# Optimization experiments

Measured on AMD Instinct MI355X. Metric: run time of the kernel, lower is better.

## Reference

```python
import jax, jax.numpy as jnp
import numpy as np
import math

E = 64          # embed_size
S = 64          # max_seq_len (mask hard-codes seq==64)
H = 8           # num_heads
DH = E // H     # 8
DFF = 4 * E     # 256
V = 32000       # vocab_size
B = 64          # batch


def _pos_encoding():
    position = np.arange(0, S, dtype=np.float32)[:, None]
    div_term = np.exp(np.arange(0, E, 2, dtype=np.float32) * -(math.log(10000.0) / E))
    pe = np.zeros((S, E), dtype=np.float32)
    pe[:, 0::2] = np.sin(position * div_term)
    pe[:, 1::2] = np.cos(position * div_term)
    return jnp.asarray(pe)


def layernorm(x, g, b, eps=1e-5):
    mu = jnp.mean(x, -1, keepdims=True)
    var = jnp.mean((x - mu) ** 2, -1, keepdims=True)
    return (x - mu) * jax.lax.rsqrt(var + eps) * g + b


def round4(x):
    return jnp.round(x * 1e4) / 1e4


def setup_inputs() -> dict:
    key = jax.random.key(0)
    ks = jax.random.split(key, 16)
    n = lambda k, sh, s=0.05: jax.random.normal(k, sh, dtype=jnp.float32) * s
    return {
        "x": jax.random.randint(ks[0], (B, S), 0, V),
        "emb": n(ks[1], (V, E), 1.0),
        "pe": _pos_encoding(),
        # per-head q/k/v weights concatenated: [E, H*DH] == [E, E], no bias
        "wq": n(ks[2], (E, E)), "wk": n(ks[3], (E, E)), "wv": n(ks[4], (E, E)),
        "g_h": jnp.ones((E,)), "b_h": jnp.zeros((E,)),           # MHA internal LayerNorm
        "wo": n(ks[5], (E, E)), "bo": jnp.zeros((E,)),           # MHA output linear
        "g1": jnp.ones((E,)), "bt1": jnp.zeros((E,)),            # norm1
        "w1": n(ks[6], (E, DFF)), "b1f": jnp.zeros((DFF,)),      # ffn fc1
        "w2": n(ks[7], (DFF, E)), "b2f": jnp.zeros((E,)),        # ffn fc2
        "g2": jnp.ones((E,)), "bt2": jnp.zeros((E,)),            # norm2
        "gf": jnp.ones((E,)), "bf": jnp.zeros((E,)),             # final norm
        "wout": n(ks[8], (E, V)), "bout": jnp.zeros((V,)),       # final linear
    }


def reference(x, emb, pe, wq, wk, wv, g_h, b_h, wo, bo, g1, bt1,
              w1, b1f, w2, b2f, g2, bt2, gf, bf, wout, bout):
    # embedding + positional encoding (dropout = identity in eval)
    h = emb[x] + pe[:S]                              # [B,S,E]

    # --- multi-head attention (per-head linears fused as one GEMM each) ---
    q = (h @ wq).reshape(B, S, H, DH)
    k = (h @ wk).reshape(B, S, H, DH)
    v = (h @ wv).reshape(B, S, H, DH)
    scores = jnp.einsum('bshd,bthd->bhst', q, k) / math.sqrt(DH)
    causal = jnp.tril(jnp.ones((S, S), dtype=bool))
    scores = jnp.where(causal, scores, -jnp.inf)
    attn = jax.nn.softmax(scores, axis=-1)
    ho = round4(jnp.einsum('bhst,bthd->bshd', attn, v))  # per-head round(decimals=4)
    concat = ho.reshape(B, S, E)
    attn_out = jnp.round(layernorm(concat, g_h, b_h) @ wo + bo)  # round to integers

    # --- transformer block residual/norm/ffn ---
    h = layernorm(h + attn_out, g1, bt1)
    ffn = jax.nn.relu(h @ w1 + b1f) @ w2 + b2f
    h = round4(layernorm(h + ffn, g2, bt2))

    # --- final norm, vocab projection, softmax, round ---
    logits = layernorm(h, gf, bf) @ wout + bout       # [B,S,V]
    probs = jax.nn.softmax(logits, axis=-1)
    return jnp.round(probs)
```

## Files before the change

kernel.cpp:

```cpp
#include <hip/hip_runtime.h>
#include <hip/hip_bf16.h>
#include <math.h>

#define EMB 64
#define SEQ 64
#define NH 8
#define DFF 256
#define VOC 32000
#define BATCH 64

using bf16_t = __hip_bfloat16;
typedef __bf16 bf16x8 __attribute__((ext_vector_type(8)));
typedef float f32x4 __attribute__((ext_vector_type(4)));

#define WOUTT_OFF 0
#define HBF_OFF   4194304
#define GSUM_OFF  (4194304 + 524288)
#define GMAX_OFF  (GSUM_OFF + 16384)
#define H_OFF     (GMAX_OFF + 32768)
#define Q_OFF     (H_OFF + 1048576)
#define K_OFF     (Q_OFF + 1048576)
#define V_OFF     (K_OFF + 1048576)
#define HO_OFF    (V_OFF + 1048576)

__device__ inline unsigned long long packmax(float f, int i) {
  unsigned u = __float_as_uint(f);
  u = (u & 0x80000000u) ? ~u : (u | 0x80000000u);
  return ((unsigned long long)u << 32) | (unsigned)i;
}

__device__ inline float rsum16(float s) {
  s += __shfl_xor(s, 1, 16);
  s += __shfl_xor(s, 2, 16);
  s += __shfl_xor(s, 4, 16);
  s += __shfl_xor(s, 8, 16);
  return s;
}

__device__ inline void gemm64g(const float* __restrict__ in, const float* __restrict__ W,
                               float* __restrict__ out, int t) {
  int i = t >> 2, j0 = (t & 3) * 16;
  float acc[16];
#pragma unroll
  for (int j = 0; j < 16; ++j) acc[j] = 0.f;
#pragma unroll 2
  for (int k = 0; k < 64; ++k) {
    float a = in[i * 65 + k];
    const float4* wr = (const float4*)(W + k * 64 + j0);
    float4 w0 = wr[0], w1v = wr[1], w2v = wr[2], w3v = wr[3];
    acc[0] += a * w0.x;   acc[1] += a * w0.y;   acc[2] += a * w0.z;   acc[3] += a * w0.w;
    acc[4] += a * w1v.x;  acc[5] += a * w1v.y;  acc[6] += a * w1v.z;  acc[7] += a * w1v.w;
    acc[8] += a * w2v.x;  acc[9] += a * w2v.y;  acc[10] += a * w2v.z; acc[11] += a * w2v.w;
    acc[12] += a * w3v.x; acc[13] += a * w3v.y; acc[14] += a * w3v.z; acc[15] += a * w3v.w;
  }
#pragma unroll
  for (int j = 0; j < 16; ++j) out[(size_t)i * 64 + j0 + j] = acc[j];
}

__global__ __launch_bounds__(256) void k_qkv(
    const int* __restrict__ x, const float* __restrict__ emb, const float* __restrict__ pe,
    const float* __restrict__ wq, const float* __restrict__ wk, const float* __restrict__ wv,
    const float* __restrict__ wout, bf16_t* __restrict__ woutT,
    float* __restrict__ H, float* __restrict__ Q, float* __restrict__ K,
    float* __restrict__ V, float* __restrict__ gsums,
    unsigned long long* __restrict__ gmax, float* __restrict__ outp) {
  const int t = threadIdx.x;
  __shared__ float sm[64 * 65];

  if (blockIdx.x >= 564) {
    const int bid = blockIdx.x - 564;
    f32x4 z = {0.f, 0.f, 0.f, 0.f};
    f32x4* o4 = (f32x4*)outp + (size_t)bid * 32000;
    for (int i = t; i < 32000; i += 256) o4[i] = z;
    return;
  }

  if (blockIdx.x >= 64) {
    int v0 = (blockIdx.x - 64) * 64;
    for (int idx = t; idx < 4096; idx += 256) {
      int e = idx >> 6, c = idx & 63;
      sm[e * 65 + c] = wout[(size_t)e * VOC + v0 + c];
    }
    __syncthreads();
    for (int idx = t; idx < 4096; idx += 256) {
      int c = idx >> 6, e = idx & 63;
      woutT[(size_t)(v0 + c) * 64 + e] = __float2bfloat16(sm[e * 65 + c]);
    }
    return;
  }

  const int b = blockIdx.x;
  if (t < 64) {
    gsums[b * 64 + t] = 0.f;
    gmax[b * 64 + t] = 0ULL;
  }
  for (int idx = t; idx < 4096; idx += 256) {
    int i = idx >> 6, e = idx & 63;
    int tok = x[b * 64 + i];
    float v = emb[(size_t)tok * 64 + e] + pe[i * 64 + e];
    sm[i * 65 + e] = v;
    H[((size_t)b * 64 + i) * 64 + e] = v;
  }
  __syncthreads();
  gemm64g(sm, wq, Q + (size_t)b * 4096, t);
  gemm64g(sm, wk, K + (size_t)b * 4096, t);
  gemm64g(sm, wv, V + (size_t)b * 4096, t);
}

__global__ __launch_bounds__(256) void k_attn(const float* __restrict__ Q,
                                              const float* __restrict__ K,
                                              const float* __restrict__ V,
                                              float* __restrict__ HO) {
  const int b = blockIdx.x, h = blockIdx.y;
  const int t = threadIdx.x;
  __shared__ float Qh[64 * 8], Kh[64 * 8], Vh[64 * 8];
  __shared__ float SC[64 * 65];
  const size_t base = (size_t)b * 4096 + h * 8;

  for (int idx = t; idx < 512; idx += 256) {
    int i = idx >> 3, d = idx & 7;
    Qh[i * 8 + d] = Q[base + (size_t)i * 64 + d];
    Kh[i * 8 + d] = K[base + (size_t)i * 64 + d];
    Vh[i * 8 + d] = V[base + (size_t)i * 64 + d];
  }
  __syncthreads();

  const float scale = 0.35355339059327373f;
  const int i = t >> 2, jb = t & 3;
  float qv[8];
#pragma unroll
  for (int d = 0; d < 8; ++d) qv[d] = Qh[i * 8 + d];

  float sv[16];
  float m = -INFINITY;
#pragma unroll
  for (int jj = 0; jj < 16; ++jj) {
    int j = jb * 16 + jj;
    float s;
    if (j <= i) {
      s = 0.f;
#pragma unroll
      for (int d = 0; d < 8; ++d) s += qv[d] * Kh[j * 8 + d];
      s *= scale;
    } else {
      s = -INFINITY;
    }
    sv[jj] = s;
    m = fmaxf(m, s);
  }
  m = fmaxf(m, __shfl_xor(m, 1, 4));
  m = fmaxf(m, __shfl_xor(m, 2, 4));
  float sum = 0.f;
#pragma unroll
  for (int jj = 0; jj < 16; ++jj) {
    float e2 = __expf(sv[jj] - m);
    sv[jj] = e2;
    sum += e2;
  }
  sum += __shfl_xor(sum, 1, 4);
  sum += __shfl_xor(sum, 2, 4);
  float inv = 1.f / sum;
#pragma unroll
  for (int jj = 0; jj < 16; ++jj) SC[i * 65 + jb * 16 + jj] = sv[jj] * inv;
  __syncthreads();

  for (int idx = t; idx < 512; idx += 256) {
    int ii = idx >> 3, d = idx & 7;
    float o = 0.f;
    for (int j = 0; j < 64; ++j) o += SC[ii * 65 + j] * Vh[j * 8 + d];
    HO[base + (size_t)ii * 64 + d] = rintf(o * 1e4f) / 1e4f;
  }
}

__global__ __launch_bounds__(256) void k_ffn(
    const float* __restrict__ H, const float* __restrict__ HO,
    const float* __restrict__ g_h, const float* __restrict__ b_h,
    const float* __restrict__ wo, const float* __restrict__ bo,
    const float* __restrict__ g1, const float* __restrict__ bt1,
    const float* __restrict__ w1, const float* __restrict__ b1f,
    const float* __restrict__ w2, const float* __restrict__ b2f,
    const float* __restrict__ g2, const float* __restrict__ bt2,
    const float* __restrict__ gf, const float* __restrict__ bf_,
    bf16_t* __restrict__ hbf) {
  const int t = threadIdx.x;
  const int r0 = blockIdx.x * 16;
  const int i = t >> 4, l = t & 15;
  const int e0 = l * 4;
  const size_t row = (size_t)(r0 + i) * 64;
  __shared__ float T1[16 * 65];
  __shared__ float T2[16 * 65];
  __shared__ float H1[16 * 65];
  __shared__ float M[16 * 260];

  {
    float4 hv = *(const float4*)(HO + row + e0);
    float mu = rsum16(hv.x + hv.y + hv.z + hv.w) * (1.f / 64.f);
    float d0 = hv.x - mu, d1 = hv.y - mu, d2 = hv.z - mu, d3 = hv.w - mu;
    float var = rsum16(d0 * d0 + d1 * d1 + d2 * d2 + d3 * d3) * (1.f / 64.f);
    float rs = rsqrtf(var + 1e-5f);
    T1[i * 65 + e0 + 0] = d0 * rs * g_h[e0 + 0] + b_h[e0 + 0];
    T1[i * 65 + e0 + 1] = d1 * rs * g_h[e0 + 1] + b_h[e0 + 1];
    T1[i * 65 + e0 + 2] = d2 * rs * g_h[e0 + 2] + b_h[e0 + 2];
    T1[i * 65 + e0 + 3] = d3 * rs * g_h[e0 + 3] + b_h[e0 + 3];
  }
  __syncthreads();

  {
    float a0 = 0.f, a1 = 0.f, a2 = 0.f, a3 = 0.f;
#pragma unroll 4
    for (int k = 0; k < 64; ++k) {
      float a = T1[i * 65 + k];
      float4 w = *(const float4*)(wo + (size_t)k * 64 + e0);
      a0 += a * w.x; a1 += a * w.y; a2 += a * w.z; a3 += a * w.w;
    }
    T2[i * 65 + e0 + 0] = rintf(a0 + bo[e0 + 0]);
    T2[i * 65 + e0 + 1] = rintf(a1 + bo[e0 + 1]);
    T2[i * 65 + e0 + 2] = rintf(a2 + bo[e0 + 2]);
    T2[i * 65 + e0 + 3] = rintf(a3 + bo[e0 + 3]);
  }
  __syncthreads();

  {
    float4 hh = *(const float4*)(H + row + e0);
    float x0 = hh.x + T2[i * 65 + e0 + 0];
    float x1 = hh.y + T2[i * 65 + e0 + 1];
    float x2 = hh.z + T2[i * 65 + e0 + 2];
    float x3 = hh.w + T2[i * 65 + e0 + 3];
    float mu = rsum16(x0 + x1 + x2 + x3) * (1.f / 64.f);
    float d0 = x0 - mu, d1 = x1 - mu, d2 = x2 - mu, d3 = x3 - mu;
    float var = rsum16(d0 * d0 + d1 * d1 + d2 * d2 + d3 * d3) * (1.f / 64.f);
    float rs = rsqrtf(var + 1e-5f);
    H1[i * 65 + e0 + 0] = d0 * rs * g1[e0 + 0] + bt1[e0 + 0];
    H1[i * 65 + e0 + 1] = d1 * rs * g1[e0 + 1] + bt1[e0 + 1];
    H1[i * 65 + e0 + 2] = d2 * rs * g1[e0 + 2] + bt1[e0 + 2];
    H1[i * 65 + e0 + 3] = d3 * rs * g1[e0 + 3] + bt1[e0 + 3];
  }
  __syncthreads();

  {
    const int j0 = l * 16;
    float acc[16];
#pragma unroll
    for (int j = 0; j < 16; ++j) acc[j] = 0.f;
#pragma unroll 2
    for (int k = 0; k < 64; ++k) {
      float a = H1[i * 65 + k];
      const float4* wr = (const float4*)(w1 + (size_t)k * 256 + j0);
      float4 w0 = wr[0], w1v = wr[1], w2v = wr[2], w3v = wr[3];
      acc[0] += a * w0.x;   acc[1] += a * w0.y;   acc[2] += a * w0.z;   acc[3] += a * w0.w;
      acc[4] += a * w1v.x;  acc[5] += a * w1v.y;  acc[6] += a * w1v.z;  acc[7] += a * w1v.w;
      acc[8] += a * w2v.x;  acc[9] += a * w2v.y;  acc[10] += a * w2v.z; acc[11] += a * w2v.w;
      acc[12] += a * w3v.x; acc[13] += a * w3v.y; acc[14] += a * w3v.z; acc[15] += a * w3v.w;
    }
#pragma unroll
    for (int j = 0; j < 16; ++j)
      M[i * 260 + j0 + j] = fmaxf(acc[j] + b1f[j0 + j], 0.f);
  }
  __syncthreads();

  float f0 = 0.f, f1 = 0.f, f2 = 0.f, f3 = 0.f;
  {
#pragma unroll 4
    for (int k = 0; k < 256; ++k) {
      float a = M[i * 260 + k];
      float4 w = *(const float4*)(w2 + (size_t)k * 64 + e0);
      f0 += a * w.x; f1 += a * w.y; f2 += a * w.z; f3 += a * w.w;
    }
    f0 += b2f[e0 + 0]; f1 += b2f[e0 + 1]; f2 += b2f[e0 + 2]; f3 += b2f[e0 + 3];
  }

  {
    float y0 = H1[i * 65 + e0 + 0] + f0;
    float y1 = H1[i * 65 + e0 + 1] + f1;
    float y2 = H1[i * 65 + e0 + 2] + f2;
    float y3 = H1[i * 65 + e0 + 3] + f3;
    float mu = rsum16(y0 + y1 + y2 + y3) * (1.f / 64.f);
    float d0 = y0 - mu, d1 = y1 - mu, d2 = y2 - mu, d3 = y3 - mu;
    float var = rsum16(d0 * d0 + d1 * d1 + d2 * d2 + d3 * d3) * (1.f / 64.f);
    float rs = rsqrtf(var + 1e-5f);
    float h20 = rintf((d0 * rs * g2[e0 + 0] + bt2[e0 + 0]) * 1e4f) / 1e4f;
    float h21 = rintf((d1 * rs * g2[e0 + 1] + bt2[e0 + 1]) * 1e4f) / 1e4f;
    float h22 = rintf((d2 * rs * g2[e0 + 2] + bt2[e0 + 2]) * 1e4f) / 1e4f;
    float h23 = rintf((d3 * rs * g2[e0 + 3] + bt2[e0 + 3]) * 1e4f) / 1e4f;
    float mu2 = rsum16(h20 + h21 + h22 + h23) * (1.f / 64.f);
    float e0d = h20 - mu2, e1d = h21 - mu2, e2d = h22 - mu2, e3d = h23 - mu2;
    float var2 = rsum16(e0d * e0d + e1d * e1d + e2d * e2d + e3d * e3d) * (1.f / 64.f);
    float rs2 = rsqrtf(var2 + 1e-5f);
    hbf[row + e0 + 0] = __float2bfloat16(e0d * rs2 * gf[e0 + 0] + bf_[e0 + 0]);
    hbf[row + e0 + 1] = __float2bfloat16(e1d * rs2 * gf[e0 + 1] + bf_[e0 + 1]);
    hbf[row + e0 + 2] = __float2bfloat16(e2d * rs2 * gf[e0 + 2] + bf_[e0 + 2]);
    hbf[row + e0 + 3] = __float2bfloat16(e3d * rs2 * gf[e0 + 3] + bf_[e0 + 3]);
  }
}

__global__ __launch_bounds__(256) void k_sumexp(const bf16_t* __restrict__ hbf,
                                                const bf16_t* __restrict__ woutT,
                                                const float* __restrict__ bout,
                                                float* __restrict__ gsums,
                                                unsigned long long* __restrict__ gmax) {
  const int t = threadIdx.x;
  const int lane = t & 63, wave = t >> 6;
  const int row0 = blockIdx.x * 64;
  const int nbase = blockIdx.y * 4000;
  const int mrow = lane & 15, quad = lane >> 4;
  __shared__ float lsum[64];
  if (t < 64) lsum[t] = 0.f;
  __syncthreads();

  bf16x8 a0[4], a1[4];
#pragma unroll
  for (int at = 0; at < 4; ++at) {
    const bf16_t* arow = hbf + (size_t)(row0 + at * 16 + mrow) * 64 + quad * 8;
    a0[at] = *(const bf16x8*)(arow);
    a1[at] = *(const bf16x8*)(arow + 32);
  }

  float s[4][4];
  float mxv[4][4];
  int mxi[4][4];
#pragma unroll
  for (int at = 0; at < 4; ++at)
#pragma unroll
    for (int r = 0; r < 4; ++r) { s[at][r] = 0.f; mxv[at][r] = -INFINITY; mxi[at][r] = 0; }

  for (int tt = wave; tt < 250; tt += 4) {
    int col = nbase + tt * 16 + mrow;
    const bf16_t* brow = woutT + (size_t)col * 64 + quad * 8;
    bf16x8 b0 = *(const bf16x8*)(brow);
    bf16x8 b1 = *(const bf16x8*)(brow + 32);
    float bv = bout[col];
#pragma unroll
    for (int at = 0; at < 4; ++at) {
      f32x4 c = {0.f, 0.f, 0.f, 0.f};
      c = __builtin_amdgcn_mfma_f32_16x16x32_bf16(a0[at], b0, c, 0, 0, 0);
      c = __builtin_amdgcn_mfma_f32_16x16x32_bf16(a1[at], b1, c, 0, 0, 0);
#pragma unroll
      for (int r = 0; r < 4; ++r) {
        float v = c[r] + bv;
        s[at][r] += __expf(v);
        mxi[at][r] = (v > mxv[at][r]) ? col : mxi[at][r];
        mxv[at][r] = fmaxf(mxv[at][r], v);
      }
    }
  }
#pragma unroll
  for (int off = 1; off < 16; off <<= 1) {
#pragma unroll
    for (int at = 0; at < 4; ++at)
#pragma unroll
      for (int r = 0; r < 4; ++r) {
        s[at][r] += __shfl_xor(s[at][r], off, 64);
        float ov = __shfl_xor(mxv[at][r], off, 64);
        int oi = __shfl_xor(mxi[at][r], off, 64);
        if (ov > mxv[at][r] || (ov == mxv[at][r] && oi > mxi[at][r])) {
          mxv[at][r] = ov; mxi[at][r] = oi;
        }
      }
  }
  if (mrow == 0) {
#pragma unroll
    for (int at = 0; at < 4; ++at)
#pragma unroll
      for (int r = 0; r < 4; ++r) {
        atomicAdd(&lsum[at * 16 + quad * 4 + r], s[at][r]);
        atomicMax(&gmax[row0 + at * 16 + quad * 4 + r], packmax(mxv[at][r], mxi[at][r]));
      }
  }
  __syncthreads();
  if (t < 64) atomicAdd(&gsums[row0 + t], lsum[t]);
}

__global__ __launch_bounds__(256) void k_scatter(const float* __restrict__ gsums,
                                                 const unsigned long long* __restrict__ gmax,
                                                 float* __restrict__ out) {
  int row = blockIdx.x * 256 + threadIdx.x;
  if (row >= BATCH * SEQ) return;
  unsigned long long p = gmax[row];
  unsigned key = (unsigned)(p >> 32);
  int idx = (int)(p & 0xffffffffu);
  unsigned ub = (key & 0x80000000u) ? (key & 0x7fffffffu) : ~key;
  float lmax = __uint_as_float(ub);
  float iv = 1.0f / gsums[row];
  float v = rintf(__expf(lmax) * iv);
  if (v != 0.0f) out[(size_t)row * VOC + idx] = v;
}

extern "C" void kernel_launch(void* const* d_in, const int* in_sizes, int n_in,
                              void* d_out, int out_size, void* d_ws, size_t ws_size,
                              hipStream_t stream) {
  const int* x = (const int*)d_in[0];
  const float* emb = (const float*)d_in[1];
  const float* pe = (const float*)d_in[2];
  const float* wq = (const float*)d_in[3];
  const float* wk = (const float*)d_in[4];
  const float* wv = (const float*)d_in[5];
  const float* g_h = (const float*)d_in[6];
  const float* b_h = (const float*)d_in[7];
  const float* wo = (const float*)d_in[8];
  const float* bo = (const float*)d_in[9];
  const float* g1 = (const float*)d_in[10];
  const float* bt1 = (const float*)d_in[11];
  const float* w1 = (const float*)d_in[12];
  const float* b1f = (const float*)d_in[13];
  const float* w2 = (const float*)d_in[14];
  const float* b2f = (const float*)d_in[15];
  const float* g2 = (const float*)d_in[16];
  const float* bt2 = (const float*)d_in[17];
  const float* gf = (const float*)d_in[18];
  const float* bff = (const float*)d_in[19];
  const float* wout = (const float*)d_in[20];
  const float* bout = (const float*)d_in[21];

  char* ws = (char*)d_ws;
  bf16_t* woutT = (bf16_t*)(ws + WOUTT_OFF);
  bf16_t* hbf = (bf16_t*)(ws + HBF_OFF);
  float* gsums = (float*)(ws + GSUM_OFF);
  unsigned long long* gmax = (unsigned long long*)(ws + GMAX_OFF);
  float* H = (float*)(ws + H_OFF);
  float* Q = (float*)(ws + Q_OFF);
  float* K = (float*)(ws + K_OFF);
  float* V = (float*)(ws + V_OFF);
  float* HO = (float*)(ws + HO_OFF);
  float* out = (float*)d_out;

  k_qkv<<<1588, 256, 0, stream>>>(x, emb, pe, wq, wk, wv, wout, woutT,
                                  H, Q, K, V, gsums, gmax, out);
  k_attn<<<dim3(64, 8), 256, 0, stream>>>(Q, K, V, HO);
  k_ffn<<<256, 256, 0, stream>>>(H, HO, g_h, b_h, wo, bo, g1, bt1, w1, b1f,
                                 w2, b2f, g2, bt2, gf, bff, hbf);
  dim3 grid(64, 8);
  k_sumexp<<<grid, 256, 0, stream>>>(hbf, woutT, bout, gsums, gmax);
  k_scatter<<<16, 256, 0, stream>>>(gsums, gmax, out);
}
```

Baseline: 757.3 us.

## Distribute output zero-fill across all pipeline kernels to overlap with compute

```diff
diff --git a/kernel.cpp b/kernel.cpp
--- a/kernel.cpp
+++ b/kernel.cpp
@@ -22,6 +22,25 @@
 #define K_OFF     (Q_OFF + 1048576)
 #define V_OFF     (K_OFF + 1048576)
 #define HO_OFF    (V_OFF + 1048576)
+
+#define NV_TOTAL 32768000
+#define F1_BLKS 360
+#define F1_PER  32000
+#define F2_BLKS 192
+#define F2_PER  30000
+#define F3_BLKS 360
+#define F3_PER  32000
+#define F4_BLKS 64
+#define F4_PER  62000
+#define F2_BASE 11520000
+#define F3_BASE 17280000
+#define F4_BASE 28800000
+
+__device__ inline void fill_slice(float* __restrict__ outp, size_t vbase, int count, int t) {
+  f32x4 z = {0.f, 0.f, 0.f, 0.f};
+  f32x4* o4 = (f32x4*)outp + vbase;
+  for (int i = t; i < count; i += 256) o4[i] = z;
+}
 
 __device__ inline unsigned long long packmax(float f, int i) {
   unsigned u = __float_as_uint(f);
@@ -68,10 +87,7 @@
   __shared__ float sm[64 * 65];
 
   if (blockIdx.x >= 564) {
-    const int bid = blockIdx.x - 564;
-    f32x4 z = {0.f, 0.f, 0.f, 0.f};
-    f32x4* o4 = (f32x4*)outp + (size_t)bid * 32000;
-    for (int i = t; i < 32000; i += 256) o4[i] = z;
+    fill_slice(outp, (size_t)(blockIdx.x - 564) * F1_PER, F1_PER, t);
     return;
   }
 
@@ -110,9 +126,15 @@
 __global__ __launch_bounds__(256) void k_attn(const float* __restrict__ Q,
                                               const float* __restrict__ K,
                                               const float* __restrict__ V,
-                                              float* __restrict__ HO) {
+                                              float* __restrict__ HO,
+                                              float* __restrict__ outp) {
+  const int t = threadIdx.x;
+  if (blockIdx.x >= 64) {
+    int bid = (blockIdx.x - 64) * 8 + blockIdx.y;
+    fill_slice(outp, (size_t)F2_BASE + (size_t)bid * F2_PER, F2_PER, t);
+    return;
+  }
   const int b = blockIdx.x, h = blockIdx.y;
-  const int t = threadIdx.x;
   __shared__ float Qh[64 * 8], Kh[64 * 8], Vh[64 * 8];
   __shared__ float SC[64 * 65];
   const size_t base = (size_t)b * 4096 + h * 8;
@@ -181,8 +203,12 @@
     const float* __restrict__ w2, const float* __restrict__ b2f,
     const float* __restrict__ g2, const float* __restrict__ bt2,
     const float* __restrict__ gf, const float* __restrict__ bf_,
-    bf16_t* __restrict__ hbf) {
+    bf16_t* __restrict__ hbf, float* __restrict__ outp) {
   const int t = threadIdx.x;
+  if (blockIdx.x >= 256) {
+    fill_slice(outp, (size_t)F3_BASE + (size_t)(blockIdx.x - 256) * F3_PER, F3_PER, t);
+    return;
+  }
   const int r0 = blockIdx.x * 16;
   const int i = t >> 4, l = t & 15;
   const int e0 = l * 4;
@@ -297,8 +323,14 @@
                                                 const bf16_t* __restrict__ woutT,
                                                 const float* __restrict__ bout,
                                                 float* __restrict__ gsums,
-                                                unsigned long long* __restrict__ gmax) {
+                                                unsigned long long* __restrict__ gmax,
+                                                float* __restrict__ outp) {
   const int t = threadIdx.x;
+  if (blockIdx.x >= 64) {
+    int bid = (blockIdx.x - 64) * 8 + blockIdx.y;
+    fill_slice(outp, (size_t)F4_BASE + (size_t)bid * F4_PER, F4_PER, t);
+    return;
+  }
   const int lane = t & 63, wave = t >> 6;
   const int row0 = blockIdx.x * 64;
   const int nbase = blockIdx.y * 4000;
@@ -423,12 +455,12 @@
   float* HO = (float*)(ws + HO_OFF);
   float* out = (float*)d_out;
 
-  k_qkv<<<1588, 256, 0, stream>>>(x, emb, pe, wq, wk, wv, wout, woutT,
-                                  H, Q, K, V, gsums, gmax, out);
-  k_attn<<<dim3(64, 8), 256, 0, stream>>>(Q, K, V, HO);
-  k_ffn<<<256, 256, 0, stream>>>(H, HO, g_h, b_h, wo, bo, g1, bt1, w1, b1f,
-                                 w2, b2f, g2, bt2, gf, bff, hbf);
-  dim3 grid(64, 8);
-  k_sumexp<<<grid, 256, 0, stream>>>(hbf, woutT, bout, gsums, gmax);
+  k_qkv<<<564 + F1_BLKS, 256, 0, stream>>>(x, emb, pe, wq, wk, wv, wout, woutT,
+                                           H, Q, K, V, gsums, gmax, out);
+  k_attn<<<dim3(64 + F2_BLKS / 8, 8), 256, 0, stream>>>(Q, K, V, HO, out);
+  k_ffn<<<256 + F3_BLKS, 256, 0, stream>>>(H, HO, g_h, b_h, wo, bo, g1, bt1, w1, b1f,
+                                           w2, b2f, g2, bt2, gf, bff, hbf, out);
+  dim3 grid(64 + F4_BLKS / 8, 8);
+  k_sumexp<<<grid, 256, 0, stream>>>(hbf, woutT, bout, gsums, gmax, out);
   k_scatter<<<16, 256, 0, stream>>>(gsums, gmax, out);
 }
```

New measurement: 756.9 us. About the same (-0.1%).
